# Performance work log

Hardware: AMD Instinct MI355X
Metric: run time of the kernel (lower is better)

The kernel has to match this reference:

```python
import jax, jax.numpy as jnp
import numpy as np

D_MODEL = 1024
D_FF = 4096
NUM_EXPERTS = 8
NUM_SLOTS = 2
LN_EPS = 1e-5


def setup_inputs() -> dict:
    key = jax.random.key(0)
    ks = jax.random.split(key, 4)
    x = jax.random.normal(ks[0], (4, 4096, D_MODEL), dtype=jnp.float32)
    slot_embeds = jax.random.normal(ks[1], (NUM_EXPERTS * NUM_SLOTS, D_MODEL), dtype=jnp.float32) * 0.02
    # per-expert MLP weights, stacked over expert axis (Linear bias=False)
    W1 = jax.random.normal(ks[2], (NUM_EXPERTS, D_MODEL, D_FF), dtype=jnp.float32) * (1.0 / np.sqrt(D_MODEL))
    W2 = jax.random.normal(ks[3], (NUM_EXPERTS, D_FF, D_MODEL), dtype=jnp.float32) * (1.0 / np.sqrt(D_FF))
    ln_gamma = jnp.ones((D_MODEL,), dtype=jnp.float32)
    ln_beta = jnp.zeros((D_MODEL,), dtype=jnp.float32)
    return {"x": x, "slot_embeds": slot_embeds, "W1": W1, "W2": W2,
            "ln_gamma": ln_gamma, "ln_beta": ln_beta}


def reference(x, slot_embeds, W1, W2, ln_gamma, ln_beta):
    B, T, D = x.shape
    E, S = NUM_EXPERTS, NUM_SLOTS
    # logits: [B, T, E*S]
    logits = jnp.einsum('btd,nd->btn', x, slot_embeds) / jnp.sqrt(jnp.asarray(D, x.dtype))
    # dispatch: softmax over tokens (dim=1)
    dispatch = jax.nn.softmax(logits, axis=1)
    slot_in = jnp.einsum('btn,btd->bnd', dispatch, x)  # [B, E*S, D]
    # LayerNorm over last dim
    mu = jnp.mean(slot_in, axis=-1, keepdims=True)
    var = jnp.mean(jnp.square(slot_in - mu), axis=-1, keepdims=True)
    h = (slot_in - mu) * jax.lax.rsqrt(var + LN_EPS) * ln_gamma + ln_beta
    # per-expert MLP as a single batched (grouped) GEMM pair
    h = h.reshape(B, E, S, D)
    u = jax.nn.gelu(jnp.einsum('besd,edf->besf', h, W1), approximate=False)
    slot_out = jnp.einsum('besf,efd->besd', u, W2).reshape(B, E * S, D)
    # combine: softmax over slots (dim=2)
    combine = jax.nn.softmax(logits, axis=2)
    return jnp.einsum('btn,bnd->btd', combine, slot_out)
```

## Files before the change

kernel.cpp:

```cpp
#include <hip/hip_runtime.h>
#include <math.h>

#define NB 4
#define NT 4096
#define ND 1024
#define NS 16
#define NE 8
#define NF 4096

__device__ __forceinline__ float gelu(float v) {
  return 0.5f * v * (1.f + erff(v * 0.70710678118654752f));
}
__device__ __forceinline__ void fma4(float4& a, float s, const float4& v) {
  a.x += s * v.x; a.y += s * v.y; a.z += s * v.z; a.w += s * v.w;
}
__device__ __forceinline__ float4 ld4(const float* p) {
  return *reinterpret_cast<const float4*>(p);
}

__global__ __launch_bounds__(256) void k_logits(const float* __restrict__ x,
                                                const float* __restrict__ se,
                                                float* __restrict__ logits) {
  __shared__ float s_se[NS * ND];
  for (int i = threadIdx.x; i < NS * ND; i += 256) s_se[i] = se[i];
  __syncthreads();
  const int wave = threadIdx.x >> 6, lane = threadIdx.x & 63;
  const int tbase = blockIdx.x * 64 + wave * 16;
  for (int g = 0; g < 4; ++g) {
    const int t0 = tbase + g * 4;
    float acc[4][NS];
#pragma unroll
    for (int tt = 0; tt < 4; ++tt)
#pragma unroll
      for (int n = 0; n < NS; ++n) acc[tt][n] = 0.f;
#pragma unroll
    for (int it = 0; it < 4; ++it) {
      const int d = it * 256 + lane * 4;
      float4 xv[4];
#pragma unroll
      for (int tt = 0; tt < 4; ++tt)
        xv[tt] = ld4(x + (size_t)(t0 + tt) * ND + d);
#pragma unroll
      for (int n = 0; n < NS; ++n) {
        const float4 sv = ld4(&s_se[n * ND + d]);
#pragma unroll
        for (int tt = 0; tt < 4; ++tt)
          acc[tt][n] += xv[tt].x * sv.x + xv[tt].y * sv.y + xv[tt].z * sv.z + xv[tt].w * sv.w;
      }
    }
#pragma unroll
    for (int tt = 0; tt < 4; ++tt)
#pragma unroll
      for (int n = 0; n < NS; ++n) {
        float v = acc[tt][n];
#pragma unroll
        for (int off = 32; off > 0; off >>= 1) v += __shfl_xor(v, off, 64);
        if (lane == n) logits[(size_t)(t0 + tt) * NS + n] = v * 0.03125f;
      }
  }
}

__global__ __launch_bounds__(256) void k_softmax_stats(const float* __restrict__ logits,
                                                       float* __restrict__ stats) {
  int bn = blockIdx.x;
  int b = bn >> 4, n = bn & 15;
  __shared__ float red[256];
  const float* lp = logits + ((size_t)b * NT) * NS + n;
  float m = -1e30f;
  for (int t = threadIdx.x; t < NT; t += 256) m = fmaxf(m, lp[(size_t)t * NS]);
  red[threadIdx.x] = m; __syncthreads();
  for (int s = 128; s > 0; s >>= 1) {
    if (threadIdx.x < s) red[threadIdx.x] = fmaxf(red[threadIdx.x], red[threadIdx.x + s]);
    __syncthreads();
  }
  m = red[0]; __syncthreads();
  float sm = 0.f;
  for (int t = threadIdx.x; t < NT; t += 256) sm += expf(lp[(size_t)t * NS] - m);
  red[threadIdx.x] = sm; __syncthreads();
  for (int s = 128; s > 0; s >>= 1) {
    if (threadIdx.x < s) red[threadIdx.x] += red[threadIdx.x + s];
    __syncthreads();
  }
  if (threadIdx.x == 0) { stats[bn * 2] = m; stats[bn * 2 + 1] = red[0]; }
}

__global__ __launch_bounds__(256) void k_slot_in(const float* __restrict__ x,
                                                 const float* __restrict__ logits,
                                                 const float* __restrict__ stats,
                                                 float* __restrict__ si_part) {
  __shared__ float s_w[NS][64];
  const int tc = blockIdx.x, b = blockIdx.y;
  const int t0 = tc * 64;
  for (int i = threadIdx.x; i < NS * 64; i += 256) {
    const int n = i >> 6, t = i & 63;
    const float m = stats[(b * NS + n) * 2], s1 = stats[(b * NS + n) * 2 + 1];
    s_w[n][t] = expf(logits[((size_t)b * NT + t0 + t) * NS + n] - m) / s1;
  }
  __syncthreads();
  float4 acc[NS];
#pragma unroll
  for (int n = 0; n < NS; ++n) acc[n] = make_float4(0.f, 0.f, 0.f, 0.f);
  const int d = threadIdx.x * 4;
  for (int t = 0; t < 64; t += 4) {
    float4 xv[4];
#pragma unroll
    for (int k = 0; k < 4; ++k)
      xv[k] = ld4(x + ((size_t)b * NT + t0 + t + k) * ND + d);
#pragma unroll
    for (int n = 0; n < NS; ++n) {
      const float4 wn = ld4(&s_w[n][t]);
      fma4(acc[n], wn.x, xv[0]); fma4(acc[n], wn.y, xv[1]);
      fma4(acc[n], wn.z, xv[2]); fma4(acc[n], wn.w, xv[3]);
    }
  }
#pragma unroll
  for (int n = 0; n < NS; ++n)
    *reinterpret_cast<float4*>(si_part + (((size_t)tc * 4 + b) * NS + n) * ND + d) = acc[n];
}

__global__ __launch_bounds__(256) void k_reduce_si(const float* __restrict__ si_part,
                                                   float* __restrict__ slot_in) {
  const int i = blockIdx.x * 256 + threadIdx.x;
  const int row = i >> 10, d = i & 1023;
  const int b = row >> 4, n = row & 15;
  float sum = 0.f;
  for (int tc = 0; tc < 64; ++tc)
    sum += si_part[(((size_t)tc * 4 + b) * NS + n) * ND + d];
  slot_in[i] = sum;
}

__global__ __launch_bounds__(256) void k_layernorm(float* __restrict__ slot_in,
                                                   const float* __restrict__ gamma,
                                                   const float* __restrict__ beta) {
  int row = blockIdx.x;
  __shared__ float red[256];
  float* rp = slot_in + (size_t)row * ND;
  float v[4];
  float sum = 0.f;
#pragma unroll
  for (int j = 0; j < 4; ++j) { v[j] = rp[threadIdx.x + j * 256]; sum += v[j]; }
  red[threadIdx.x] = sum; __syncthreads();
  for (int s = 128; s > 0; s >>= 1) {
    if (threadIdx.x < s) red[threadIdx.x] += red[threadIdx.x + s];
    __syncthreads();
  }
  float mu = red[0] * (1.f / ND); __syncthreads();
  float vs = 0.f;
#pragma unroll
  for (int j = 0; j < 4; ++j) { float t = v[j] - mu; vs += t * t; }
  red[threadIdx.x] = vs; __syncthreads();
  for (int s = 128; s > 0; s >>= 1) {
    if (threadIdx.x < s) red[threadIdx.x] += red[threadIdx.x + s];
    __syncthreads();
  }
  float rstd = rsqrtf(red[0] * (1.f / ND) + 1e-5f);
#pragma unroll
  for (int j = 0; j < 4; ++j) {
    int dd = threadIdx.x + j * 256;
    rp[dd] = (v[j] - mu) * rstd * gamma[dd] + beta[dd];
  }
}

__global__ __launch_bounds__(256) void k_mlp1(const float* __restrict__ h,
                                              const float* __restrict__ W1,
                                              float* __restrict__ u_part) {
  __shared__ float s_h[64][8];
  const int ft = blockIdx.x, dc = blockIdx.y, e = blockIdx.z;
  for (int i = threadIdx.x; i < 512; i += 256) {
    const int dd = i >> 3, j = i & 7;
    const int b = j >> 1, s = j & 1;
    s_h[dd][j] = h[((size_t)b * NS + e * 2 + s) * ND + dc * 64 + dd];
  }
  __syncthreads();
  float4 acc[8];
#pragma unroll
  for (int j = 0; j < 8; ++j) acc[j] = make_float4(0.f, 0.f, 0.f, 0.f);
  const int f = ft * 1024 + threadIdx.x * 4;
  const float* wbase = W1 + ((size_t)e * ND + dc * 64) * NF + f;
  for (int dd = 0; dd < 64; dd += 4) {
    float4 wv[4];
#pragma unroll
    for (int k = 0; k < 4; ++k)
      wv[k] = ld4(wbase + (size_t)(dd + k) * NF);
#pragma unroll
    for (int k = 0; k < 4; ++k) {
      const float4 h0 = ld4(&s_h[dd + k][0]);
      const float4 h1 = ld4(&s_h[dd + k][4]);
      fma4(acc[0], h0.x, wv[k]); fma4(acc[1], h0.y, wv[k]);
      fma4(acc[2], h0.z, wv[k]); fma4(acc[3], h0.w, wv[k]);
      fma4(acc[4], h1.x, wv[k]); fma4(acc[5], h1.y, wv[k]);
      fma4(acc[6], h1.z, wv[k]); fma4(acc[7], h1.w, wv[k]);
    }
  }
#pragma unroll
  for (int j = 0; j < 8; ++j) {
    const int b = j >> 1, s = j & 1;
    const size_t row = ((size_t)b * NE + e) * 2 + s;
    *reinterpret_cast<float4*>(u_part + ((size_t)dc * 64 + row) * NF + f) = acc[j];
  }
}

__global__ __launch_bounds__(256) void k_reduce_gelu(const float* __restrict__ u_part,
                                                     float* __restrict__ u) {
  const int i = blockIdx.x * 256 + threadIdx.x;
  float sum = 0.f;
  for (int dc = 0; dc < 16; ++dc)
    sum += u_part[(size_t)dc * 262144 + i];
  u[i] = gelu(sum);
}

__global__ __launch_bounds__(256) void k_mlp2(const float* __restrict__ u,
                                              const float* __restrict__ W2,
                                              float* __restrict__ so_part) {
  __shared__ float s_u[64][8];
  const int fc = blockIdx.x, e = blockIdx.y;
  for (int i = threadIdx.x; i < 512; i += 256) {
    const int ff = i >> 3, j = i & 7;
    const int b = j >> 1, s = j & 1;
    s_u[ff][j] = u[(((size_t)b * NE + e) * 2 + s) * NF + fc * 64 + ff];
  }
  __syncthreads();
  float4 acc[8];
#pragma unroll
  for (int j = 0; j < 8; ++j) acc[j] = make_float4(0.f, 0.f, 0.f, 0.f);
  const int d = threadIdx.x * 4;
  const float* wbase = W2 + ((size_t)e * NF + fc * 64) * ND + d;
  for (int ff = 0; ff < 64; ff += 4) {
    float4 wv[4];
#pragma unroll
    for (int k = 0; k < 4; ++k)
      wv[k] = ld4(wbase + (size_t)(ff + k) * ND);
#pragma unroll
    for (int k = 0; k < 4; ++k) {
      const float4 u0 = ld4(&s_u[ff + k][0]);
      const float4 u1 = ld4(&s_u[ff + k][4]);
      fma4(acc[0], u0.x, wv[k]); fma4(acc[1], u0.y, wv[k]);
      fma4(acc[2], u0.z, wv[k]); fma4(acc[3], u0.w, wv[k]);
      fma4(acc[4], u1.x, wv[k]); fma4(acc[5], u1.y, wv[k]);
      fma4(acc[6], u1.z, wv[k]); fma4(acc[7], u1.w, wv[k]);
    }
  }
#pragma unroll
  for (int j = 0; j < 8; ++j) {
    const int b = j >> 1, s = j & 1;
    const size_t row = (size_t)b * NS + e * 2 + s;
    *reinterpret_cast<float4*>(so_part + ((size_t)fc * 64 + row) * ND + d) = acc[j];
  }
}

__global__ __launch_bounds__(256) void k_reduce_so(const float* __restrict__ so_part,
                                                   float* __restrict__ slot_out) {
  const int i = blockIdx.x * 256 + threadIdx.x;
  float sum = 0.f;
  for (int fc = 0; fc < 64; ++fc)
    sum += so_part[(size_t)fc * 65536 + i];
  slot_out[i] = sum;
}

__global__ __launch_bounds__(256) void k_combine(const float* __restrict__ logits,
                                                 const float* __restrict__ slot_out,
                                                 float* __restrict__ out) {
  __shared__ float s_so[NS * ND];
  const int tb = blockIdx.x, b = blockIdx.y;
  for (int i = threadIdx.x; i < NS * ND; i += 256)
    s_so[i] = slot_out[(size_t)b * NS * ND + i];
  __syncthreads();
  const int wave = threadIdx.x >> 6, lane = threadIdx.x & 63;
  const int tbase = tb * 64 + wave * 16;
  for (int g = 0; g < 4; ++g) {
    const int t0 = tbase + g * 4;
    float c[4][NS];
#pragma unroll
    for (int tt = 0; tt < 4; ++tt) {
      const float* lp = logits + ((size_t)b * NT + t0 + tt) * NS;
      float l[NS];
      float m = -1e30f;
#pragma unroll
      for (int n = 0; n < NS; ++n) { l[n] = lp[n]; m = fmaxf(m, l[n]); }
      float s = 0.f;
#pragma unroll
      for (int n = 0; n < NS; ++n) { l[n] = expf(l[n] - m); s += l[n]; }
      const float rs = 1.f / s;
#pragma unroll
      for (int n = 0; n < NS; ++n) c[tt][n] = l[n] * rs;
    }
#pragma unroll
    for (int it = 0; it < 4; ++it) {
      const int d = it * 256 + lane * 4;
      float4 acc[4];
#pragma unroll
      for (int tt = 0; tt < 4; ++tt) acc[tt] = make_float4(0.f, 0.f, 0.f, 0.f);
#pragma unroll
      for (int n = 0; n < NS; ++n) {
        const float4 sv = ld4(&s_so[n * ND + d]);
        fma4(acc[0], c[0][n], sv); fma4(acc[1], c[1][n], sv);
        fma4(acc[2], c[2][n], sv); fma4(acc[3], c[3][n], sv);
      }
#pragma unroll
      for (int tt = 0; tt < 4; ++tt)
        *reinterpret_cast<float4*>(out + ((size_t)b * NT + t0 + tt) * ND + d) = acc[tt];
    }
  }
}

extern "C" void kernel_launch(void* const* d_in, const int* in_sizes, int n_in,
                              void* d_out, int out_size, void* d_ws, size_t ws_size,
                              hipStream_t stream) {
  const float* x     = (const float*)d_in[0];
  const float* se    = (const float*)d_in[1];
  const float* W1    = (const float*)d_in[2];
  const float* W2    = (const float*)d_in[3];
  const float* gamma = (const float*)d_in[4];
  const float* beta  = (const float*)d_in[5];
  float* out = (float*)d_out;

  float* ws       = (float*)d_ws;
  float* logits   = ws;
  float* stats    = ws + 262144;
  float* slot_in  = ws + 262400;
  float* slot_out = ws + 327936;
  float* u        = ws + 393472;
  float* si_part  = ws + 655616;
  float* u_part   = ws + 4849920;
  float* so_part  = ws + 9044224;

  k_logits<<<256, 256, 0, stream>>>(x, se, logits);
  k_softmax_stats<<<NB * NS, 256, 0, stream>>>(logits, stats);
  k_slot_in<<<dim3(64, NB), 256, 0, stream>>>(x, logits, stats, si_part);
  k_reduce_si<<<256, 256, 0, stream>>>(si_part, slot_in);
  k_layernorm<<<NB * NS, 256, 0, stream>>>(slot_in, gamma, beta);
  k_mlp1<<<dim3(4, 16, NE), 256, 0, stream>>>(slot_in, W1, u_part);
  k_reduce_gelu<<<1024, 256, 0, stream>>>(u_part, u);
  k_mlp2<<<dim3(64, NE), 256, 0, stream>>>(u, W2, so_part);
  k_reduce_so<<<256, 256, 0, stream>>>(so_part, slot_out);
  k_combine<<<dim3(64, NB), 256, 0, stream>>>(logits, slot_out, out);
}
```

Before: 475.8 us.

## Split MLP GEMV K across block halves, prefetch loads, restructure logits reduction

```diff
diff --git a/kernel.cpp b/kernel.cpp
--- a/kernel.cpp
+++ b/kernel.cpp
@@ -18,46 +18,43 @@
   return *reinterpret_cast<const float4*>(p);
 }
 
-__global__ __launch_bounds__(256) void k_logits(const float* __restrict__ x,
-                                                const float* __restrict__ se,
-                                                float* __restrict__ logits) {
-  __shared__ float s_se[NS * ND];
-  for (int i = threadIdx.x; i < NS * ND; i += 256) s_se[i] = se[i];
-  __syncthreads();
+__global__ __launch_bounds__(256, 4) void k_logits(const float* __restrict__ x,
+                                                   const float* __restrict__ se,
+                                                   float* __restrict__ logits) {
   const int wave = threadIdx.x >> 6, lane = threadIdx.x & 63;
-  const int tbase = blockIdx.x * 64 + wave * 16;
-  for (int g = 0; g < 4; ++g) {
-    const int t0 = tbase + g * 4;
-    float acc[4][NS];
+  const int t0 = blockIdx.x * 16 + wave * 4;
+  float acc[64];
+#pragma unroll
+  for (int j = 0; j < 64; ++j) acc[j] = 0.f;
+  for (int it = 0; it < 4; ++it) {
+    const int d = it * 256 + lane * 4;
+    float4 xv[4];
 #pragma unroll
     for (int tt = 0; tt < 4; ++tt)
-#pragma unroll
-      for (int n = 0; n < NS; ++n) acc[tt][n] = 0.f;
-#pragma unroll
-    for (int it = 0; it < 4; ++it) {
-      const int d = it * 256 + lane * 4;
-      float4 xv[4];
-#pragma unroll
-      for (int tt = 0; tt < 4; ++tt)
-        xv[tt] = ld4(x + (size_t)(t0 + tt) * ND + d);
-#pragma unroll
-      for (int n = 0; n < NS; ++n) {
-        const float4 sv = ld4(&s_se[n * ND + d]);
-#pragma unroll
-        for (int tt = 0; tt < 4; ++tt)
-          acc[tt][n] += xv[tt].x * sv.x + xv[tt].y * sv.y + xv[tt].z * sv.z + xv[tt].w * sv.w;
+      xv[tt] = ld4(x + (size_t)(t0 + tt) * ND + d);
+#pragma unroll
+    for (int n = 0; n < NS; ++n) {
+      const float4 sv = ld4(se + (size_t)n * ND + d);
+#pragma unroll
+      for (int tt = 0; tt < 4; ++tt) {
+        acc[tt * 16 + n] += xv[tt].x * sv.x + xv[tt].y * sv.y +
+                            xv[tt].z * sv.z + xv[tt].w * sv.w;
       }
     }
-#pragma unroll
-    for (int tt = 0; tt < 4; ++tt)
-#pragma unroll
-      for (int n = 0; n < NS; ++n) {
-        float v = acc[tt][n];
-#pragma unroll
-        for (int off = 32; off > 0; off >>= 1) v += __shfl_xor(v, off, 64);
-        if (lane == n) logits[(size_t)(t0 + tt) * NS + n] = v * 0.03125f;
-      }
-  }
+  }
+#pragma unroll
+  for (int k = 0; k < 6; ++k) {
+    const int dlt = 1 << k;
+    const bool hi = (lane & dlt) != 0;
+#pragma unroll
+    for (int i = 0; i < (64 >> (k + 1)); ++i) {
+      const float a = acc[2 * i], b = acc[2 * i + 1];
+      const float send = hi ? a : b;
+      const float recv = __shfl_xor(send, dlt, 64);
+      acc[i] = (hi ? b : a) + recv;
+    }
+  }
+  logits[(size_t)t0 * NS + lane] = acc[0] * 0.03125f;
 }
 
 __global__ __launch_bounds__(256) void k_softmax_stats(const float* __restrict__ logits,
@@ -101,16 +98,26 @@
 #pragma unroll
   for (int n = 0; n < NS; ++n) acc[n] = make_float4(0.f, 0.f, 0.f, 0.f);
   const int d = threadIdx.x * 4;
-  for (int t = 0; t < 64; t += 4) {
-    float4 xv[4];
-#pragma unroll
-    for (int k = 0; k < 4; ++k)
-      xv[k] = ld4(x + ((size_t)b * NT + t0 + t + k) * ND + d);
+  const float* xb = x + ((size_t)b * NT + t0) * ND + d;
+  float4 xv[2][8];
+#pragma unroll
+  for (int k = 0; k < 8; ++k) xv[0][k] = ld4(xb + (size_t)k * ND);
+#pragma unroll
+  for (int g = 0; g < 8; ++g) {
+    const int cur = g & 1;
+    if (g < 7) {
+#pragma unroll
+      for (int k = 0; k < 8; ++k)
+        xv[cur ^ 1][k] = ld4(xb + (size_t)((g + 1) * 8 + k) * ND);
+    }
 #pragma unroll
     for (int n = 0; n < NS; ++n) {
-      const float4 wn = ld4(&s_w[n][t]);
-      fma4(acc[n], wn.x, xv[0]); fma4(acc[n], wn.y, xv[1]);
-      fma4(acc[n], wn.z, xv[2]); fma4(acc[n], wn.w, xv[3]);
+      const float4 w0 = ld4(&s_w[n][g * 8]);
+      const float4 w1 = ld4(&s_w[n][g * 8 + 4]);
+      fma4(acc[n], w0.x, xv[cur][0]); fma4(acc[n], w0.y, xv[cur][1]);
+      fma4(acc[n], w0.z, xv[cur][2]); fma4(acc[n], w0.w, xv[cur][3]);
+      fma4(acc[n], w1.x, xv[cur][4]); fma4(acc[n], w1.y, xv[cur][5]);
+      fma4(acc[n], w1.z, xv[cur][6]); fma4(acc[n], w1.w, xv[cur][7]);
     }
   }
 #pragma unroll
@@ -161,42 +168,60 @@
   }
 }
 
-__global__ __launch_bounds__(256) void k_mlp1(const float* __restrict__ h,
-                                              const float* __restrict__ W1,
-                                              float* __restrict__ u_part) {
+__global__ __launch_bounds__(512, 4) void k_mlp1(const float* __restrict__ h,
+                                                 const float* __restrict__ W1,
+                                                 float* __restrict__ u_part) {
   __shared__ float s_h[64][8];
+  __shared__ float4 s_red[8][256];
   const int ft = blockIdx.x, dc = blockIdx.y, e = blockIdx.z;
-  for (int i = threadIdx.x; i < 512; i += 256) {
-    const int dd = i >> 3, j = i & 7;
+  {
+    const int dd = threadIdx.x >> 3, j = threadIdx.x & 7;
     const int b = j >> 1, s = j & 1;
     s_h[dd][j] = h[((size_t)b * NS + e * 2 + s) * ND + dc * 64 + dd];
   }
   __syncthreads();
+  const int tid = threadIdx.x & 255, half = threadIdx.x >> 8;
   float4 acc[8];
 #pragma unroll
   for (int j = 0; j < 8; ++j) acc[j] = make_float4(0.f, 0.f, 0.f, 0.f);
-  const int f = ft * 1024 + threadIdx.x * 4;
-  const float* wbase = W1 + ((size_t)e * ND + dc * 64) * NF + f;
-  for (int dd = 0; dd < 64; dd += 4) {
-    float4 wv[4];
-#pragma unroll
-    for (int k = 0; k < 4; ++k)
-      wv[k] = ld4(wbase + (size_t)(dd + k) * NF);
+  const int f = ft * 1024 + tid * 4;
+  const float* wb = W1 + ((size_t)e * ND + dc * 64 + half * 32) * NF + f;
+  float4 wv[2][4];
+#pragma unroll
+  for (int k = 0; k < 4; ++k) wv[0][k] = ld4(wb + (size_t)k * NF);
+#pragma unroll
+  for (int g = 0; g < 8; ++g) {
+    const int cur = g & 1;
+    if (g < 7) {
+#pragma unroll
+      for (int k = 0; k < 4; ++k)
+        wv[cur ^ 1][k] = ld4(wb + (size_t)((g + 1) * 4 + k) * NF);
+    }
 #pragma unroll
     for (int k = 0; k < 4; ++k) {
-      const float4 h0 = ld4(&s_h[dd + k][0]);
-      const float4 h1 = ld4(&s_h[dd + k][4]);
-      fma4(acc[0], h0.x, wv[k]); fma4(acc[1], h0.y, wv[k]);
-      fma4(acc[2], h0.z, wv[k]); fma4(acc[3], h0.w, wv[k]);
-      fma4(acc[4], h1.x, wv[k]); fma4(acc[5], h1.y, wv[k]);
-      fma4(acc[6], h1.z, wv[k]); fma4(acc[7], h1.w, wv[k]);
-    }
-  }
-#pragma unroll
-  for (int j = 0; j < 8; ++j) {
-    const int b = j >> 1, s = j & 1;
-    const size_t row = ((size_t)b * NE + e) * 2 + s;
-    *reinterpret_cast<float4*>(u_part + ((size_t)dc * 64 + row) * NF + f) = acc[j];
+      const int dd = half * 32 + g * 4 + k;
+      const float4 h0 = ld4(&s_h[dd][0]);
+      const float4 h1 = ld4(&s_h[dd][4]);
+      fma4(acc[0], h0.x, wv[cur][k]); fma4(acc[1], h0.y, wv[cur][k]);
+      fma4(acc[2], h0.z, wv[cur][k]); fma4(acc[3], h0.w, wv[cur][k]);
+      fma4(acc[4], h1.x, wv[cur][k]); fma4(acc[5], h1.y, wv[cur][k]);
+      fma4(acc[6], h1.z, wv[cur][k]); fma4(acc[7], h1.w, wv[cur][k]);
+    }
+  }
+  if (half == 1) {
+#pragma unroll
+    for (int j = 0; j < 8; ++j) s_red[j][tid] = acc[j];
+  }
+  __syncthreads();
+  if (half == 0) {
+#pragma unroll
+    for (int j = 0; j < 8; ++j) {
+      const float4 o = s_red[j][tid];
+      acc[j].x += o.x; acc[j].y += o.y; acc[j].z += o.z; acc[j].w += o.w;
+      const int b = j >> 1, s = j & 1;
+      const size_t row = ((size_t)b * NE + e) * 2 + s;
+      *reinterpret_cast<float4*>(u_part + ((size_t)dc * 64 + row) * NF + f) = acc[j];
+    }
   }
 }
 
@@ -209,42 +234,60 @@
   u[i] = gelu(sum);
 }
 
-__global__ __launch_bounds__(256) void k_mlp2(const float* __restrict__ u,
-                                              const float* __restrict__ W2,
-                                              float* __restrict__ so_part) {
+__global__ __launch_bounds__(512, 4) void k_mlp2(const float* __restrict__ u,
+                                                 const float* __restrict__ W2,
+                                                 float* __restrict__ so_part) {
   __shared__ float s_u[64][8];
+  __shared__ float4 s_red[8][256];
   const int fc = blockIdx.x, e = blockIdx.y;
-  for (int i = threadIdx.x; i < 512; i += 256) {
-    const int ff = i >> 3, j = i & 7;
+  {
+    const int ff = threadIdx.x >> 3, j = threadIdx.x & 7;
     const int b = j >> 1, s = j & 1;
     s_u[ff][j] = u[(((size_t)b * NE + e) * 2 + s) * NF + fc * 64 + ff];
   }
   __syncthreads();
+  const int tid = threadIdx.x & 255, half = threadIdx.x >> 8;
   float4 acc[8];
 #pragma unroll
   for (int j = 0; j < 8; ++j) acc[j] = make_float4(0.f, 0.f, 0.f, 0.f);
-  const int d = threadIdx.x * 4;
-  const float* wbase = W2 + ((size_t)e * NF + fc * 64) * ND + d;
-  for (int ff = 0; ff < 64; ff += 4) {
-    float4 wv[4];
-#pragma unroll
-    for (int k = 0; k < 4; ++k)
-      wv[k] = ld4(wbase + (size_t)(ff + k) * ND);
+  const int d = tid * 4;
+  const float* wb = W2 + ((size_t)e * NF + fc * 64 + half * 32) * ND + d;
+  float4 wv[2][4];
+#pragma unroll
+  for (int k = 0; k < 4; ++k) wv[0][k] = ld4(wb + (size_t)k * ND);
+#pragma unroll
+  for (int g = 0; g < 8; ++g) {
+    const int cur = g & 1;
+    if (g < 7) {
+#pragma unroll
+      for (int k = 0; k < 4; ++k)
+        wv[cur ^ 1][k] = ld4(wb + (size_t)((g + 1) * 4 + k) * ND);
+    }
 #pragma unroll
     for (int k = 0; k < 4; ++k) {
-      const float4 u0 = ld4(&s_u[ff + k][0]);
-      const float4 u1 = ld4(&s_u[ff + k][4]);
-      fma4(acc[0], u0.x, wv[k]); fma4(acc[1], u0.y, wv[k]);
-      fma4(acc[2], u0.z, wv[k]); fma4(acc[3], u0.w, wv[k]);
-      fma4(acc[4], u1.x, wv[k]); fma4(acc[5], u1.y, wv[k]);
-      fma4(acc[6], u1.z, wv[k]); fma4(acc[7], u1.w, wv[k]);
-    }
-  }
-#pragma unroll
-  for (int j = 0; j < 8; ++j) {
-    const int b = j >> 1, s = j & 1;
-    const size_t row = (size_t)b * NS + e * 2 + s;
-    *reinterpret_cast<float4*>(so_part + ((size_t)fc * 64 + row) * ND + d) = acc[j];
+      const int ff = half * 32 + g * 4 + k;
+      const float4 u0 = ld4(&s_u[ff][0]);
+      const float4 u1 = ld4(&s_u[ff][4]);
+      fma4(acc[0], u0.x, wv[cur][k]); fma4(acc[1], u0.y, wv[cur][k]);
+      fma4(acc[2], u0.z, wv[cur][k]); fma4(acc[3], u0.w, wv[cur][k]);
+      fma4(acc[4], u1.x, wv[cur][k]); fma4(acc[5], u1.y, wv[cur][k]);
+      fma4(acc[6], u1.z, wv[cur][k]); fma4(acc[7], u1.w, wv[cur][k]);
+    }
+  }
+  if (half == 1) {
+#pragma unroll
+    for (int j = 0; j < 8; ++j) s_red[j][tid] = acc[j];
+  }
+  __syncthreads();
+  if (half == 0) {
+#pragma unroll
+    for (int j = 0; j < 8; ++j) {
+      const float4 o = s_red[j][tid];
+      acc[j].x += o.x; acc[j].y += o.y; acc[j].z += o.z; acc[j].w += o.w;
+      const int b = j >> 1, s = j & 1;
+      const size_t row = (size_t)b * NS + e * 2 + s;
+      *reinterpret_cast<float4*>(so_part + ((size_t)fc * 64 + row) * ND + d) = acc[j];
+    }
   }
 }
 
@@ -324,14 +367,14 @@
   float* u_part   = ws + 4849920;
   float* so_part  = ws + 9044224;
 
-  k_logits<<<256, 256, 0, stream>>>(x, se, logits);
+  k_logits<<<1024, 256, 0, stream>>>(x, se, logits);
   k_softmax_stats<<<NB * NS, 256, 0, stream>>>(logits, stats);
   k_slot_in<<<dim3(64, NB), 256, 0, stream>>>(x, logits, stats, si_part);
   k_reduce_si<<<256, 256, 0, stream>>>(si_part, slot_in);
   k_layernorm<<<NB * NS, 256, 0, stream>>>(slot_in, gamma, beta);
-  k_mlp1<<<dim3(4, 16, NE), 256, 0, stream>>>(slot_in, W1, u_part);
+  k_mlp1<<<dim3(4, 16, NE), 512, 0, stream>>>(slot_in, W1, u_part);
   k_reduce_gelu<<<1024, 256, 0, stream>>>(u_part, u);
-  k_mlp2<<<dim3(64, NE), 256, 0, stream>>>(u, W2, so_part);
+  k_mlp2<<<dim3(64, NE), 512, 0, stream>>>(u, W2, so_part);
   k_reduce_so<<<256, 256, 0, stream>>>(so_part, slot_out);
   k_combine<<<dim3(64, NB), 256, 0, stream>>>(logits, slot_out, out);
 }
```

Result: no change. 469.1 us (-1.4%).
